# Optimization experiments

Measured on AMD Instinct MI355X. Metric: run time of the kernel, lower is better.

Reference implementation:

```python
import jax, jax.numpy as jnp
import numpy as np

N_NODES = 170000
N_EDGES = 1200000
IN_C, HID_C, OUT_C = 128, 128, 40
BN_EPS = 1e-5


def setup_inputs() -> dict:
    key = jax.random.key(0)
    ks = jax.random.split(key, 12)
    def glorot(k, fan_in, fan_out):
        lim = (6.0 / (fan_in + fan_out)) ** 0.5
        return jax.random.uniform(k, (fan_in, fan_out), jnp.float32, -lim, lim)
    x = jax.random.normal(ks[0], (N_NODES, IN_C), jnp.float32)
    edge_index = jax.random.randint(ks[1], (2, N_EDGES), 0, N_NODES, jnp.int64)
    return {
        "x": x,
        "edge_index": edge_index,
        "W0": glorot(ks[2], IN_C, HID_C), "b0": jnp.zeros((HID_C,), jnp.float32),
        "g0": jnp.ones((HID_C,), jnp.float32), "be0": jnp.zeros((HID_C,), jnp.float32),
        "W1": glorot(ks[3], HID_C, HID_C), "b1": jnp.zeros((HID_C,), jnp.float32),
        "g1": jnp.ones((HID_C,), jnp.float32), "be1": jnp.zeros((HID_C,), jnp.float32),
        "W2": glorot(ks[4], HID_C, OUT_C), "b2": jnp.zeros((OUT_C,), jnp.float32),
    }


def _gcn_norm(edge_index, num_nodes):
    # add self-loops, symmetric normalization (PyG GCNConv default)
    loop = jnp.arange(num_nodes, dtype=edge_index.dtype)
    src = jnp.concatenate([edge_index[0], loop])
    dst = jnp.concatenate([edge_index[1], loop])
    deg = jax.ops.segment_sum(jnp.ones_like(dst, jnp.float32), dst, num_segments=num_nodes)
    dinv = jnp.where(deg > 0, jax.lax.rsqrt(deg), 0.0)
    norm = dinv[src] * dinv[dst]  # [E+N]
    return src, dst, norm


def _conv(h, W, b, src, dst, norm, num_nodes):
    h = h @ W                              # [N, out]
    msg = h[src] * norm[:, None]           # gather + scale, [E+N, out]
    out = jax.ops.segment_sum(msg, dst, num_segments=num_nodes)
    return out + b


def _bn_relu(h, g, be):
    mean = jnp.mean(h, axis=0)
    var = jnp.mean(jnp.square(h - mean), axis=0)  # biased, as torch BN training
    h = (h - mean) * jax.lax.rsqrt(var + BN_EPS) * g + be
    return jax.nn.relu(h)


def reference(x, edge_index, W0, b0, g0, be0, W1, b1, g1, be1, W2, b2):
    N = x.shape[0]
    src, dst, norm = _gcn_norm(edge_index, N)
    h = _bn_relu(_conv(x, W0, b0, src, dst, norm, N), g0, be0)
    h = _bn_relu(_conv(h, W1, b1, src, dst, norm, N), g1, be1)
    return _conv(h, W2, b2, src, dst, norm, N)
```

## Files before the change

kernel.cpp:

```cpp
#include <hip/hip_runtime.h>

#define BN_EPS 1e-5f
#define CAP 3072

using bf16x8 = __attribute__((ext_vector_type(8))) short;
using f32x4  = __attribute__((ext_vector_type(4))) float;

__device__ __forceinline__ unsigned int f2bf(float f) {
    unsigned int u = __float_as_uint(f);
    u += 0x7fffu + ((u >> 16) & 1u);
    return u >> 16;
}
__device__ __forceinline__ unsigned int f2bf2(float lo, float hi) {
    unsigned int r;
    asm("v_cvt_pk_bf16_f32 %0, %1, %2" : "=v"(r) : "v"(lo), "v"(hi));
    return r;
}
__device__ __forceinline__ float bflo(unsigned int u) { return __uint_as_float(u << 16); }
__device__ __forceinline__ float bfhi(unsigned int u) { return __uint_as_float(u & 0xffff0000u); }

__global__ __launch_bounds__(256) void k_prepW3(const float* __restrict__ W0,
                                                const float* __restrict__ W1,
                                                const float* __restrict__ W2,
                                                unsigned short* __restrict__ Wf,
                                                int* __restrict__ bcur,
                                                float* __restrict__ stats, int NB) {
    int t = blockIdx.x * 256 + threadIdx.x;
    if (t < NB) bcur[t] = t * CAP;
    if (t < 512) stats[t] = 0.f;
    int wid = t >> 11;
    int f = t & 2047;
    const float* W = (wid == 0) ? W0 : (wid == 1) ? W1 : W2;
    int C = (wid == 2) ? 40 : 128;
    int lane = f & 63, frag = f >> 6;
    int kt = frag & 3, ct = frag >> 2;
    int r = lane & 15, q = lane >> 4;
    int col = ct * 16 + r;
    int kbase = kt * 32 + q * 8;
    unsigned int v[8];
    #pragma unroll
    for (int j = 0; j < 8; ++j)
        v[j] = (col < C) ? f2bf(W[(size_t)(kbase + j) * C + col]) : 0u;
    uint4 o;
    o.x = v[0] | (v[1] << 16);
    o.y = v[2] | (v[3] << 16);
    o.z = v[4] | (v[5] << 16);
    o.w = v[6] | (v[7] << 16);
    ((uint4*)Wf)[t] = o;
}

__global__ __launch_bounds__(256) void k_bscatter(const int* __restrict__ ei,
                                                  int* __restrict__ bcur,
                                                  unsigned int* __restrict__ ebuf,
                                                  int E, int NB) {
    __shared__ int h[768];
    __shared__ int wb[768];
    for (int i = threadIdx.x; i < 768; i += 256) h[i] = 0;
    __syncthreads();
    int base = blockIdx.x * 8192;
    int rk[32];
    #pragma unroll
    for (int it = 0; it < 32; ++it) {
        int e = base + it * 256 + threadIdx.x;
        rk[it] = (e < E) ? atomicAdd(&h[ei[E + e] >> 8], 1) : 0;
    }
    __syncthreads();
    for (int i = threadIdx.x; i < NB; i += 256) {
        int c = h[i];
        wb[i] = c ? atomicAdd(&bcur[i], c) : 0;
    }
    __syncthreads();
    #pragma unroll
    for (int it = 0; it < 32; ++it) {
        int e = base + it * 256 + threadIdx.x;
        if (e < E) {
            unsigned s = (unsigned)ei[e], d = (unsigned)ei[E + e];
            int bk = (int)(d >> 8);
            int pos = wb[bk] + rk[it];
            if (pos >= bk * CAP && pos < (bk + 1) * CAP)
                ebuf[pos] = s | ((d & 255u) << 24);
        }
    }
}

__global__ __launch_bounds__(256) void k_final_gemm0(
        const unsigned int* __restrict__ ebuf, const int* __restrict__ bcur,
        int* __restrict__ csr, int* __restrict__ rs, int* __restrict__ re,
        float* __restrict__ dinv,
        const float* __restrict__ X, const unsigned short* __restrict__ Wf,
        unsigned short* __restrict__ H, int N, int NB) {
    __shared__ int cnt[256];
    __shared__ int scn[256];
    __shared__ int cur[256];
    __shared__ unsigned short bF[8 * 4 * 512];
    const int t = threadIdx.x;
    if (blockIdx.x < (unsigned)NB) {
        const int b = blockIdx.x;
        const int beg = b * CAP;
        const int cntE = min(bcur[b] - beg, CAP);
        cnt[t] = 0;
        __syncthreads();
        for (int j = t; j < cntE; j += 256)
            atomicAdd(&cnt[ebuf[beg + j] >> 24], 1);
        __syncthreads();
        int v = cnt[t];
        scn[t] = v;
        __syncthreads();
        for (int off = 1; off < 256; off <<= 1) {
            int x = (t >= off) ? scn[t - off] : 0;
            __syncthreads();
            scn[t] += x;
            __syncthreads();
        }
        int excl = scn[t] - v;
        int node = b * 256 + t;
        if (node < N) {
            rs[node]   = beg + excl;
            re[node]   = beg + excl + v;
            dinv[node] = rsqrtf((float)(1 + v));
        }
        cur[t] = beg + excl;
        __syncthreads();
        for (int j = t; j < cntE; j += 256) {
            unsigned e = ebuf[beg + j];
            int pos = atomicAdd(&cur[e >> 24], 1);
            csr[pos] = (int)(e & 0x00FFFFFFu);
        }
        return;
    }
    const int rowbase = (blockIdx.x - NB) * 64;
    {
        const uint4* src = (const uint4*)Wf;
        uint4* dst = (uint4*)bF;
        #pragma unroll
        for (int i = 0; i < 8; ++i) dst[t + 256 * i] = src[t + 256 * i];
    }
    __syncthreads();

    const int wave = t >> 6, lane = t & 63;
    const int r = lane & 15, q = lane >> 4;
    const int row  = rowbase + wave * 16 + r;
    const int rowc = min(row, N - 1);

    bf16x8 afr[4];
    #pragma unroll
    for (int kt = 0; kt < 4; ++kt) {
        const int kc = kt * 32 + q * 8;
        const float4* xp = (const float4*)(X + (size_t)rowc * 128 + kc);
        float4 p0 = xp[0], p1 = xp[1];
        union { unsigned int u[4]; bf16x8 v; } pk;
        pk.u[0] = f2bf2(p0.x, p0.y);
        pk.u[1] = f2bf2(p0.z, p0.w);
        pk.u[2] = f2bf2(p1.x, p1.y);
        pk.u[3] = f2bf2(p1.z, p1.w);
        afr[kt] = pk.v;
    }

    f32x4 acc[8];
    #pragma unroll
    for (int ct = 0; ct < 8; ++ct) acc[ct] = (f32x4){0.f, 0.f, 0.f, 0.f};
    #pragma unroll
    for (int kt = 0; kt < 4; ++kt) {
        #pragma unroll
        for (int ct = 0; ct < 8; ++ct) {
            bf16x8 b = ((const bf16x8*)bF)[(ct * 4 + kt) * 64 + lane];
            acc[ct] = __builtin_amdgcn_mfma_f32_16x16x32_bf16(afr[kt], b, acc[ct], 0, 0, 0);
        }
    }
    #pragma unroll
    for (int ct = 0; ct < 8; ++ct) {
        #pragma unroll
        for (int i = 0; i < 4; i += 2) {
            int row0 = rowbase + wave * 16 + q * 4 + i;
            unsigned int pk = f2bf2(acc[ct][i], acc[ct][i + 1]);
            if (row0 < N)
                H[(size_t)row0 * 128 + ct * 16 + r] = (unsigned short)pk;
            if (row0 + 1 < N)
                H[(size_t)(row0 + 1) * 128 + ct * 16 + r] = (unsigned short)(pk >> 16);
        }
    }
}

template <int NOCT, int OST>
__global__ __launch_bounds__(256) void k_gemm_mfma(
        const unsigned short* __restrict__ X, const unsigned short* __restrict__ Wf,
        unsigned short* __restrict__ H, int N,
        const float* __restrict__ stats, const float* __restrict__ g,
        const float* __restrict__ be) {
    __shared__ unsigned short bF[NOCT * 4 * 512];
    __shared__ float2 bnss[128];
    const int tid = threadIdx.x;
    const int rowbase = blockIdx.x * 64;

    if (tid < 128) {
        const float invN = 1.0f / (float)N;
        float mean = stats[tid] * invN;
        float var  = fmaf(-mean, mean, stats[128 + tid] * invN);
        float sc   = g[tid] * rsqrtf(var + BN_EPS);
        bnss[tid]  = make_float2(sc, fmaf(-mean, sc, be[tid]));
    }
    {
        const uint4* src = (const uint4*)Wf;
        uint4* dst = (uint4*)bF;
        #pragma unroll
        for (int i = 0; i < NOCT; ++i) dst[tid + 256 * i] = src[tid + 256 * i];
    }
    __syncthreads();

    const int wave = tid >> 6, lane = tid & 63;
    const int r = lane & 15, q = lane >> 4;
    const int row  = rowbase + wave * 16 + r;
    const int rowc = min(row, N - 1);

    bf16x8 afr[4];
    #pragma unroll
    for (int kt = 0; kt < 4; ++kt) {
        const int kc = kt * 32 + q * 8;
        uint4 p = *((const uint4*)(X + (size_t)rowc * 128 + kc));
        float vv[8];
        vv[0] = bflo(p.x); vv[1] = bfhi(p.x);
        vv[2] = bflo(p.y); vv[3] = bfhi(p.y);
        vv[4] = bflo(p.z); vv[5] = bfhi(p.z);
        vv[6] = bflo(p.w); vv[7] = bfhi(p.w);
        #pragma unroll
        for (int j = 0; j < 8; ++j) {
            float2 ss = bnss[kc + j];
            vv[j] = fmaxf(fmaf(vv[j], ss.x, ss.y), 0.0f);
        }
        union { unsigned int u[4]; bf16x8 v; } pk;
        pk.u[0] = f2bf2(vv[0], vv[1]);
        pk.u[1] = f2bf2(vv[2], vv[3]);
        pk.u[2] = f2bf2(vv[4], vv[5]);
        pk.u[3] = f2bf2(vv[6], vv[7]);
        afr[kt] = pk.v;
    }

    f32x4 acc[NOCT];
    #pragma unroll
    for (int ct = 0; ct < NOCT; ++ct) acc[ct] = (f32x4){0.f, 0.f, 0.f, 0.f};

    #pragma unroll
    for (int kt = 0; kt < 4; ++kt) {
        #pragma unroll
        for (int ct = 0; ct < NOCT; ++ct) {
            bf16x8 b = ((const bf16x8*)bF)[(ct * 4 + kt) * 64 + lane];
            acc[ct] = __builtin_amdgcn_mfma_f32_16x16x32_bf16(afr[kt], b, acc[ct], 0, 0, 0);
        }
    }

    #pragma unroll
    for (int ct = 0; ct < NOCT; ++ct) {
        #pragma unroll
        for (int i = 0; i < 4; i += 2) {
            int row0 = rowbase + wave * 16 + q * 4 + i;
            unsigned int pk = f2bf2(acc[ct][i], acc[ct][i + 1]);
            if (row0 < N)
                H[(size_t)row0 * OST + ct * 16 + r] = (unsigned short)pk;
            if (row0 + 1 < N)
                H[(size_t)(row0 + 1) * OST + ct * 16 + r] = (unsigned short)(pk >> 16);
        }
    }
}

__global__ __launch_bounds__(256) void k_agg128(
        const unsigned short* __restrict__ H, const int* __restrict__ rs,
        const int* __restrict__ re, const int* __restrict__ csr,
        const float* __restrict__ dinv, const float* __restrict__ b,
        unsigned short* __restrict__ outb, int N) {
    int lane = threadIdx.x & 15;
    int node = blockIdx.x * 16 + (threadIdx.x >> 4);
    if (node >= N) return;
    float dd  = dinv[node];
    int   beg = rs[node];
    int   end = re[node];
    uint4 hp  = ((const uint4*)(H + (size_t)node * 128))[lane];
    float4 bb0 = ((const float4*)b)[lane * 2];
    float4 bb1 = ((const float4*)b)[lane * 2 + 1];
    float sl = dd * dd;
    float a0 = fmaf(bflo(hp.x), sl, bb0.x), a1 = fmaf(bfhi(hp.x), sl, bb0.y);
    float a2 = fmaf(bflo(hp.y), sl, bb0.z), a3 = fmaf(bfhi(hp.y), sl, bb0.w);
    float a4 = fmaf(bflo(hp.z), sl, bb1.x), a5 = fmaf(bfhi(hp.z), sl, bb1.y);
    float a6 = fmaf(bflo(hp.w), sl, bb1.z), a7 = fmaf(bfhi(hp.w), sl, bb1.w);
    int j = beg;
    for (; j + 2 <= end; j += 2) {
        int s0 = csr[j], s1 = csr[j + 1];
        float n0 = dinv[s0] * dd, n1 = dinv[s1] * dd;
        uint4 v0 = ((const uint4*)(H + (size_t)s0 * 128))[lane];
        uint4 v1 = ((const uint4*)(H + (size_t)s1 * 128))[lane];
        a0 = fmaf(bflo(v0.x), n0, fmaf(bflo(v1.x), n1, a0));
        a1 = fmaf(bfhi(v0.x), n0, fmaf(bfhi(v1.x), n1, a1));
        a2 = fmaf(bflo(v0.y), n0, fmaf(bflo(v1.y), n1, a2));
        a3 = fmaf(bfhi(v0.y), n0, fmaf(bfhi(v1.y), n1, a3));
        a4 = fmaf(bflo(v0.z), n0, fmaf(bflo(v1.z), n1, a4));
        a5 = fmaf(bfhi(v0.z), n0, fmaf(bfhi(v1.z), n1, a5));
        a6 = fmaf(bflo(v0.w), n0, fmaf(bflo(v1.w), n1, a6));
        a7 = fmaf(bfhi(v0.w), n0, fmaf(bfhi(v1.w), n1, a7));
    }
    if (j < end) {
        int s0 = csr[j];
        float n0 = dinv[s0] * dd;
        uint4 v0 = ((const uint4*)(H + (size_t)s0 * 128))[lane];
        a0 = fmaf(bflo(v0.x), n0, a0); a1 = fmaf(bfhi(v0.x), n0, a1);
        a2 = fmaf(bflo(v0.y), n0, a2); a3 = fmaf(bfhi(v0.y), n0, a3);
        a4 = fmaf(bflo(v0.z), n0, a4); a5 = fmaf(bfhi(v0.z), n0, a5);
        a6 = fmaf(bflo(v0.w), n0, a6); a7 = fmaf(bfhi(v0.w), n0, a7);
    }
    uint4 o;
    o.x = f2bf2(a0, a1);
    o.y = f2bf2(a2, a3);
    o.z = f2bf2(a4, a5);
    o.w = f2bf2(a6, a7);
    ((uint4*)(outb + (size_t)node * 128))[lane] = o;
}

__global__ __launch_bounds__(256) void k_agg40(
        const unsigned short* __restrict__ H, const int* __restrict__ rs,
        const int* __restrict__ re, const int* __restrict__ csr,
        const float* __restrict__ dinv, const float* __restrict__ b,
        float* __restrict__ out, int N) {
    int lane = threadIdx.x & 15;
    int node = blockIdx.x * 16 + (threadIdx.x >> 4);
    if (node >= N || lane >= 10) return;
    float dd  = dinv[node];
    int   beg = rs[node];
    int   end = re[node];
    uint2 hp  = ((const uint2*)(H + (size_t)node * 64))[lane];
    float4 bb = ((const float4*)b)[lane];
    float  sl = dd * dd;
    float4 acc = make_float4(fmaf(bflo(hp.x), sl, bb.x), fmaf(bfhi(hp.x), sl, bb.y),
                             fmaf(bflo(hp.y), sl, bb.z), fmaf(bfhi(hp.y), sl, bb.w));
    int j = beg;
    for (; j + 2 <= end; j += 2) {
        int s0 = csr[j], s1 = csr[j + 1];
        float n0 = dinv[s0] * dd, n1 = dinv[s1] * dd;
        uint2 v0 = ((const uint2*)(H + (size_t)s0 * 64))[lane];
        uint2 v1 = ((const uint2*)(H + (size_t)s1 * 64))[lane];
        acc.x = fmaf(bflo(v0.x), n0, fmaf(bflo(v1.x), n1, acc.x));
        acc.y = fmaf(bfhi(v0.x), n0, fmaf(bfhi(v1.x), n1, acc.y));
        acc.z = fmaf(bflo(v0.y), n0, fmaf(bflo(v1.y), n1, acc.z));
        acc.w = fmaf(bfhi(v0.y), n0, fmaf(bfhi(v1.y), n1, acc.w));
    }
    if (j < end) {
        int s0 = csr[j];
        float n0 = dinv[s0] * dd;
        uint2 v0 = ((const uint2*)(H + (size_t)s0 * 64))[lane];
        acc.x = fmaf(bflo(v0.x), n0, acc.x);
        acc.y = fmaf(bfhi(v0.x), n0, acc.y);
        acc.z = fmaf(bflo(v0.y), n0, acc.z);
        acc.w = fmaf(bfhi(v0.y), n0, acc.w);
    }
    ((float4*)(out + (size_t)node * 40))[lane] = acc;
}

__global__ __launch_bounds__(256) void k_bnstats(
        const unsigned short* __restrict__ Bb, float* __restrict__ stats, int N) {
    __shared__ float red[2][16][128];
    const int t = threadIdx.x;
    const int lane16 = t & 15, grp = t >> 4;
    const int cbase = lane16 * 8;
    float s[8], q[8];
    #pragma unroll
    for (int k = 0; k < 8; ++k) { s[k] = 0.f; q[k] = 0.f; }

    const int step = gridDim.x * 16;
    for (int r = blockIdx.x * 16 + grp; r < N; r += 2 * step) {
        uint4 p0 = *((const uint4*)(Bb + (size_t)r * 128 + cbase));
        int r1 = r + step;
        if (r1 < N) {
            uint4 p1 = *((const uint4*)(Bb + (size_t)r1 * 128 + cbase));
            float v[8] = {bflo(p1.x), bfhi(p1.x), bflo(p1.y), bfhi(p1.y),
                          bflo(p1.z), bfhi(p1.z), bflo(p1.w), bfhi(p1.w)};
            #pragma unroll
            for (int k = 0; k < 8; ++k) { s[k] += v[k]; q[k] = fmaf(v[k], v[k], q[k]); }
        }
        float u[8] = {bflo(p0.x), bfhi(p0.x), bflo(p0.y), bfhi(p0.y),
                      bflo(p0.z), bfhi(p0.z), bflo(p0.w), bfhi(p0.w)};
        #pragma unroll
        for (int k = 0; k < 8; ++k) { s[k] += u[k]; q[k] = fmaf(u[k], u[k], q[k]); }
    }
    #pragma unroll
    for (int k = 0; k < 8; ++k) {
        red[0][grp][cbase + k] = s[k];
        red[1][grp][cbase + k] = q[k];
    }
    __syncthreads();
    if (t < 128) {
        float acc = 0.f;
        #pragma unroll
        for (int g = 0; g < 16; ++g) acc += red[0][g][t];
        unsafeAtomicAdd(&stats[t], acc);
    } else {
        int c = t - 128;
        float acc = 0.f;
        #pragma unroll
        for (int g = 0; g < 16; ++g) acc += red[1][g][c];
        unsafeAtomicAdd(&stats[128 + c], acc);
    }
}

extern "C" void kernel_launch(void* const* d_in, const int* in_sizes, int n_in,
                              void* d_out, int out_size, void* d_ws, size_t ws_size,
                              hipStream_t stream) {
    const float* x   = (const float*)d_in[0];
    const int*   ei  = (const int*)d_in[1];
    const float* W0  = (const float*)d_in[2];
    const float* b0  = (const float*)d_in[3];
    const float* g0  = (const float*)d_in[4];
    const float* be0 = (const float*)d_in[5];
    const float* W1  = (const float*)d_in[6];
    const float* b1  = (const float*)d_in[7];
    const float* g1  = (const float*)d_in[8];
    const float* be1 = (const float*)d_in[9];
    const float* W2  = (const float*)d_in[10];
    const float* b2  = (const float*)d_in[11];
    float* out = (float*)d_out;

    const int N  = in_sizes[0] / 128;
    const int E  = in_sizes[1] / 2;
    const int NB = (N + 255) >> 8;
    const int EB = (E + 8191) / 8192;

    float* ws   = (float*)d_ws;
    size_t Npad = ((size_t)N + 511) & ~(size_t)511;
    size_t BCAP = (size_t)NB * CAP;
    float* dinv = ws;
    int*   rs   = (int*)(ws + Npad);
    int*   re   = rs + Npad;
    int*   csr  = re + Npad;
    unsigned int* ebuf = (unsigned int*)(csr + BCAP);
    int*   bcur = (int*)(ebuf + BCAP);
    float* stats0 = (float*)(bcur + 1024);
    float* stats1 = stats0 + 256;
    unsigned short* Wf = (unsigned short*)(stats1 + 256);
    unsigned short* Hb = Wf + 3 * 16384;
    unsigned short* Bb = Hb + Npad * 128;

    int gemm_grid = (N + 63) / 64;
    int agg_grid  = (N + 15) / 16;

    k_prepW3  <<<24, 256, 0, stream>>>(W0, W1, W2, Wf, bcur, stats0, NB);
    k_bscatter<<<EB, 256, 0, stream>>>(ei, bcur, ebuf, E, NB);
    k_final_gemm0<<<NB + gemm_grid, 256, 0, stream>>>(ebuf, bcur, csr, rs, re,
                                                      dinv, x, Wf, Hb, N, NB);

    k_agg128<<<agg_grid, 256, 0, stream>>>(Hb, rs, re, csr, dinv, b0, Bb, N);
    k_bnstats<<<512, 256, 0, stream>>>(Bb, stats0, N);

    k_gemm_mfma<8, 128><<<gemm_grid, 256, 0, stream>>>(Bb, Wf + 16384, Hb, N,
                                                       stats0, g0, be0);
    k_agg128<<<agg_grid, 256, 0, stream>>>(Hb, rs, re, csr, dinv, b1, Bb, N);
    k_bnstats<<<512, 256, 0, stream>>>(Bb, stats1, N);

    k_gemm_mfma<3, 64><<<gemm_grid, 256, 0, stream>>>(Bb, Wf + 2 * 16384, Hb, N,
                                                      stats1, g1, be1);
    k_agg40<<<agg_grid, 256, 0, stream>>>(Hb, rs, re, csr, dinv, b2, out, N);
}
```

Measured before the change: 447.5 us.

## Fuse BatchNorm statistics accumulation into the aggregation kernel

Removes the separate k_bnstats pass, which reread the full bf16 aggregated activations after each hidden layer. Each k_agg128 block now reduces its 16 nodes' fp32 sums and sums of squares in shared memory and atomically adds them into one of 8 stat slabs, with a rotated column order to spread atomic contention. The GEMM kernel sums the 8 slabs when it builds the BN scale and shift. This trades one bandwidth pass and one launch per layer for a much larger number of global atomics, one set per aggregation block, and extra shared memory plus a barrier in the aggregation kernel.

```diff
diff --git a/kernel.cpp b/kernel.cpp
--- a/kernel.cpp
+++ b/kernel.cpp
@@ -27,7 +27,7 @@
                                                 float* __restrict__ stats, int NB) {
     int t = blockIdx.x * 256 + threadIdx.x;
     if (t < NB) bcur[t] = t * CAP;
-    if (t < 512) stats[t] = 0.f;
+    if (t < 4096) stats[t] = 0.f;
     int wid = t >> 11;
     int f = t & 2047;
     const float* W = (wid == 0) ? W0 : (wid == 1) ? W1 : W2;
@@ -194,8 +194,14 @@
 
     if (tid < 128) {
         const float invN = 1.0f / (float)N;
-        float mean = stats[tid] * invN;
-        float var  = fmaf(-mean, mean, stats[128 + tid] * invN);
+        float se = 0.f, sq = 0.f;
+        #pragma unroll
+        for (int s = 0; s < 8; ++s) {
+            se += stats[s * 256 + tid];
+            sq += stats[s * 256 + 128 + tid];
+        }
+        float mean = se * invN;
+        float var  = fmaf(-mean, mean, sq * invN);
         float sc   = g[tid] * rsqrtf(var + BN_EPS);
         bnss[tid]  = make_float2(sc, fmaf(-mean, sc, be[tid]));
     }
@@ -266,14 +272,17 @@
         const unsigned short* __restrict__ H, const int* __restrict__ rs,
         const int* __restrict__ re, const int* __restrict__ csr,
         const float* __restrict__ dinv, const float* __restrict__ b,
-        unsigned short* __restrict__ outb, int N) {
-    int lane = threadIdx.x & 15;
-    int node = blockIdx.x * 16 + (threadIdx.x >> 4);
-    if (node >= N) return;
-    float dd  = dinv[node];
-    int   beg = rs[node];
-    int   end = re[node];
-    uint4 hp  = ((const uint4*)(H + (size_t)node * 128))[lane];
+        unsigned short* __restrict__ outb, float* __restrict__ stats, int N) {
+    __shared__ float red[2][16][128];
+    const int t = threadIdx.x;
+    int lane = t & 15;
+    int node = blockIdx.x * 16 + (t >> 4);
+    const bool valid = node < N;
+    const int nodec = valid ? node : 0;
+    float dd  = dinv[nodec];
+    int   beg = rs[nodec];
+    int   end = valid ? re[nodec] : beg;
+    uint4 hp  = ((const uint4*)(H + (size_t)nodec * 128))[lane];
     float4 bb0 = ((const float4*)b)[lane * 2];
     float4 bb1 = ((const float4*)b)[lane * 2 + 1];
     float sl = dd * dd;
@@ -305,12 +314,41 @@
         a4 = fmaf(bflo(v0.z), n0, a4); a5 = fmaf(bfhi(v0.z), n0, a5);
         a6 = fmaf(bflo(v0.w), n0, a6); a7 = fmaf(bfhi(v0.w), n0, a7);
     }
-    uint4 o;
-    o.x = f2bf2(a0, a1);
-    o.y = f2bf2(a2, a3);
-    o.z = f2bf2(a4, a5);
-    o.w = f2bf2(a6, a7);
-    ((uint4*)(outb + (size_t)node * 128))[lane] = o;
+    if (valid) {
+        uint4 o;
+        o.x = f2bf2(a0, a1);
+        o.y = f2bf2(a2, a3);
+        o.z = f2bf2(a4, a5);
+        o.w = f2bf2(a6, a7);
+        ((uint4*)(outb + (size_t)node * 128))[lane] = o;
+    } else {
+        a0 = a1 = a2 = a3 = a4 = a5 = a6 = a7 = 0.f;
+    }
+    const int grp = t >> 4, cb = lane * 8;
+    red[0][grp][cb + 0] = a0; red[1][grp][cb + 0] = a0 * a0;
+    red[0][grp][cb + 1] = a1; red[1][grp][cb + 1] = a1 * a1;
+    red[0][grp][cb + 2] = a2; red[1][grp][cb + 2] = a2 * a2;
+    red[0][grp][cb + 3] = a3; red[1][grp][cb + 3] = a3 * a3;
+    red[0][grp][cb + 4] = a4; red[1][grp][cb + 4] = a4 * a4;
+    red[0][grp][cb + 5] = a5; red[1][grp][cb + 5] = a5 * a5;
+    red[0][grp][cb + 6] = a6; red[1][grp][cb + 6] = a6 * a6;
+    red[0][grp][cb + 7] = a7; red[1][grp][cb + 7] = a7 * a7;
+    __syncthreads();
+    const int slab = blockIdx.x & 7;
+    const int rot  = (blockIdx.x >> 3) << 2;
+    if (t < 128) {
+        int c = (t + rot) & 127;
+        float acc = 0.f;
+        #pragma unroll
+        for (int g = 0; g < 16; ++g) acc += red[0][g][c];
+        unsafeAtomicAdd(&stats[slab * 256 + c], acc);
+    } else {
+        int c = ((t - 128) + rot) & 127;
+        float acc = 0.f;
+        #pragma unroll
+        for (int g = 0; g < 16; ++g) acc += red[1][g][c];
+        unsafeAtomicAdd(&stats[slab * 256 + 128 + c], acc);
+    }
 }
 
 __global__ __launch_bounds__(256) void k_agg40(
@@ -352,52 +390,6 @@
     ((float4*)(out + (size_t)node * 40))[lane] = acc;
 }
 
-__global__ __launch_bounds__(256) void k_bnstats(
-        const unsigned short* __restrict__ Bb, float* __restrict__ stats, int N) {
-    __shared__ float red[2][16][128];
-    const int t = threadIdx.x;
-    const int lane16 = t & 15, grp = t >> 4;
-    const int cbase = lane16 * 8;
-    float s[8], q[8];
-    #pragma unroll
-    for (int k = 0; k < 8; ++k) { s[k] = 0.f; q[k] = 0.f; }
-
-    const int step = gridDim.x * 16;
-    for (int r = blockIdx.x * 16 + grp; r < N; r += 2 * step) {
-        uint4 p0 = *((const uint4*)(Bb + (size_t)r * 128 + cbase));
-        int r1 = r + step;
-        if (r1 < N) {
-            uint4 p1 = *((const uint4*)(Bb + (size_t)r1 * 128 + cbase));
-            float v[8] = {bflo(p1.x), bfhi(p1.x), bflo(p1.y), bfhi(p1.y),
-                          bflo(p1.z), bfhi(p1.z), bflo(p1.w), bfhi(p1.w)};
-            #pragma unroll
-            for (int k = 0; k < 8; ++k) { s[k] += v[k]; q[k] = fmaf(v[k], v[k], q[k]); }
-        }
-        float u[8] = {bflo(p0.x), bfhi(p0.x), bflo(p0.y), bfhi(p0.y),
-                      bflo(p0.z), bfhi(p0.z), bflo(p0.w), bfhi(p0.w)};
-        #pragma unroll
-        for (int k = 0; k < 8; ++k) { s[k] += u[k]; q[k] = fmaf(u[k], u[k], q[k]); }
-    }
-    #pragma unroll
-    for (int k = 0; k < 8; ++k) {
-        red[0][grp][cbase + k] = s[k];
-        red[1][grp][cbase + k] = q[k];
-    }
-    __syncthreads();
-    if (t < 128) {
-        float acc = 0.f;
-        #pragma unroll
-        for (int g = 0; g < 16; ++g) acc += red[0][g][t];
-        unsafeAtomicAdd(&stats[t], acc);
-    } else {
-        int c = t - 128;
-        float acc = 0.f;
-        #pragma unroll
-        for (int g = 0; g < 16; ++g) acc += red[1][g][c];
-        unsafeAtomicAdd(&stats[128 + c], acc);
-    }
-}
-
 extern "C" void kernel_launch(void* const* d_in, const int* in_sizes, int n_in,
                               void* d_out, int out_size, void* d_ws, size_t ws_size,
                               hipStream_t stream) {
@@ -430,8 +422,8 @@
     unsigned int* ebuf = (unsigned int*)(csr + BCAP);
     int*   bcur = (int*)(ebuf + BCAP);
     float* stats0 = (float*)(bcur + 1024);
-    float* stats1 = stats0 + 256;
-    unsigned short* Wf = (unsigned short*)(stats1 + 256);
+    float* stats1 = stats0 + 2048;
+    unsigned short* Wf = (unsigned short*)(stats1 + 2048);
     unsigned short* Hb = Wf + 3 * 16384;
     unsigned short* Bb = Hb + Npad * 128;
 
@@ -443,13 +435,13 @@
     k_final_gemm0<<<NB + gemm_grid, 256, 0, stream>>>(ebuf, bcur, csr, rs, re,
                                                       dinv, x, Wf, Hb, N, NB);
 
-    k_agg128<<<agg_grid, 256, 0, stream>>>(Hb, rs, re, csr, dinv, b0, Bb, N);
-    k_bnstats<<<512, 256, 0, stream>>>(Bb, stats0, N);
+    k_agg128<<<agg_grid, 256, 0, stream>>>(Hb, rs, re, csr, dinv, b0, Bb,
+                                           stats0, N);
 
     k_gemm_mfma<8, 128><<<gemm_grid, 256, 0, stream>>>(Bb, Wf + 16384, Hb, N,
                                                        stats0, g0, be0);
-    k_agg128<<<agg_grid, 256, 0, stream>>>(Hb, rs, re, csr, dinv, b1, Bb, N);
-    k_bnstats<<<512, 256, 0, stream>>>(Bb, stats1, N);
+    k_agg128<<<agg_grid, 256, 0, stream>>>(Hb, rs, re, csr, dinv, b1, Bb,
+                                           stats1, N);
 
     k_gemm_mfma<3, 64><<<gemm_grid, 256, 0, stream>>>(Bb, Wf + 2 * 16384, Hb, N,
                                                       stats1, g1, be1);
```

Result: no change. 439.2 us (-1.8%).
